# Kernel tuning notes

Hardware: AMD Instinct MI355X
Metric: run time of the kernel (lower is better)

## Reference

```python
import jax, jax.numpy as jnp
import numpy as np

B, T, C, H = 4, 1024, 1024, 16
HS = C // H  # head_size = 64
EPS = 1e-5


def layer_norm(x, w, b):
    mu = jnp.mean(x, axis=-1, keepdims=True)
    var = jnp.mean(jnp.square(x - mu), axis=-1, keepdims=True)
    return (x - mu) * jax.lax.rsqrt(var + EPS) * w + b


def setup_inputs() -> dict:
    key = jax.random.key(0)
    ks = jax.random.split(key, 12)
    s = 0.02
    return {
        "x": jax.random.normal(ks[0], (B, T, C), jnp.float32),
        "ln1_w": jnp.ones((C,), jnp.float32),
        "ln1_b": jnp.zeros((C,), jnp.float32),
        "Wk": jax.random.normal(ks[1], (H, C, HS), jnp.float32) * s,
        "Wq": jax.random.normal(ks[2], (H, C, HS), jnp.float32) * s,
        "Wv": jax.random.normal(ks[3], (H, C, HS), jnp.float32) * s,
        "Wo": jax.random.normal(ks[4], (C, C), jnp.float32) * s,
        "bo": jnp.zeros((C,), jnp.float32),
        "ln2_w": jnp.ones((C,), jnp.float32),
        "ln2_b": jnp.zeros((C,), jnp.float32),
        "W1": jax.random.normal(ks[5], (C, 4 * C), jnp.float32) * s,
        "b1": jnp.zeros((4 * C,), jnp.float32),
        "prelu_a": jnp.asarray(0.25, jnp.float32),
        "W2": jax.random.normal(ks[6], (4 * C, C), jnp.float32) * s,
        "b2": jnp.zeros((C,), jnp.float32),
    }


def reference(x, ln1_w, ln1_b, Wk, Wq, Wv, Wo, bo, ln2_w, ln2_b, W1, b1, prelu_a, W2, b2):
    # --- self-attention branch (pre-LN) ---
    h = layer_norm(x, ln1_w, ln1_b)  # [B,T,C]
    k = jnp.einsum('btc,hcd->bhtd', h, Wk)
    q = jnp.einsum('btc,hcd->bhtd', h, Wq)
    v = jnp.einsum('btc,hcd->bhtd', h, Wv)
    # NOTE: source computes k @ q^T (not q @ k^T) scaled by n_embd**-0.5
    wei = jnp.einsum('bhtd,bhsd->bhts', k, q) * (C ** -0.5)  # [B,H,T,T]
    causal = jnp.tril(jnp.ones((T, T), bool))
    wei = jnp.where(causal, wei, -jnp.inf)
    wei = jax.nn.softmax(wei, axis=-1)
    out = jnp.einsum('bhts,bhsd->bthd', wei, v).reshape(B, T, C)
    out = out @ Wo + bo
    x = x + out
    # --- feed-forward branch (pre-LN) ---
    h2 = layer_norm(x, ln2_w, ln2_b)
    f = h2 @ W1 + b1
    f = jnp.where(f > 0, f, prelu_a * f)  # PReLU, single scalar param
    f = f @ W2 + b2
    return x + f
```

## Files before the change

kernel.cpp:

```cpp
#include <hip/hip_runtime.h>


typedef __bf16 bf16_t;
typedef __attribute__((ext_vector_type(8))) __bf16 bfx8;
typedef __attribute__((ext_vector_type(4))) __bf16 bfx4;
typedef __attribute__((ext_vector_type(4))) float f32x4;
typedef __attribute__((ext_vector_type(8))) unsigned short u16x8;
typedef unsigned int u32;

#define MFMA_BF16(a, b, c) __builtin_amdgcn_mfma_f32_16x16x32_bf16((a), (b), (c), 0, 0, 0)
#define GLOAD_LDS16(g, l)                                                     \
  __builtin_amdgcn_global_load_lds((__attribute__((address_space(1))) void*)(g), \
                                   (__attribute__((address_space(3))) void*)(l), 16, 0, 0)

__global__ __launch_bounds__(256) void ln_kernel(const float* __restrict__ x,
                                                 const float* __restrict__ w,
                                                 const float* __restrict__ b,
                                                 bf16_t* __restrict__ out) {
  const int row = blockIdx.x;
  const int tid = threadIdx.x;
  const float4 v = reinterpret_cast<const float4*>(x + (size_t)row * 1024)[tid];
  float s = v.x + v.y + v.z + v.w;
  float s2 = v.x * v.x + v.y * v.y + v.z * v.z + v.w * v.w;
#pragma unroll
  for (int off = 1; off < 64; off <<= 1) {
    s += __shfl_xor(s, off);
    s2 += __shfl_xor(s2, off);
  }
  __shared__ float red[8];
  const int wv = tid >> 6;
  if ((tid & 63) == 0) {
    red[wv] = s;
    red[4 + wv] = s2;
  }
  __syncthreads();
  s = red[0] + red[1] + red[2] + red[3];
  s2 = red[4] + red[5] + red[6] + red[7];
  const float mu = s * (1.0f / 1024.0f);
  const float rs = rsqrtf(s2 * (1.0f / 1024.0f) - mu * mu + 1e-5f);
  const float4 wv4 = reinterpret_cast<const float4*>(w)[tid];
  const float4 bv4 = reinterpret_cast<const float4*>(b)[tid];
  bfx4 o;
  o[0] = (bf16_t)((v.x - mu) * rs * wv4.x + bv4.x);
  o[1] = (bf16_t)((v.y - mu) * rs * wv4.y + bv4.y);
  o[2] = (bf16_t)((v.z - mu) * rs * wv4.z + bv4.z);
  o[3] = (bf16_t)((v.w - mu) * rs * wv4.w + bv4.w);
  reinterpret_cast<bfx4*>(out + (size_t)row * 1024)[tid] = o;
}

__device__ __forceinline__ void tc_body(const float* __restrict__ in,
                                        bf16_t* __restrict__ out, int K, int N, int k0,
                                        int n0, float (*tile)[65], int t) {
  const int rl = t >> 4, cl = (t & 15) * 4;
#pragma unroll
  for (int p = 0; p < 4; ++p) {
    const int r = p * 16 + rl;
    const float4 v = *reinterpret_cast<const float4*>(in + (size_t)(k0 + r) * N + n0 + cl);
    tile[r][cl] = v.x;
    tile[r][cl + 1] = v.y;
    tile[r][cl + 2] = v.z;
    tile[r][cl + 3] = v.w;
  }
  __syncthreads();
#pragma unroll
  for (int p = 0; p < 2; ++p) {
    const int idx = p * 256 + t;
    const int n = idx >> 3, kc = (idx & 7) * 8;
    bfx8 o;
#pragma unroll
    for (int i = 0; i < 8; ++i) o[i] = (bf16_t)tile[kc + i][n];
    *reinterpret_cast<bfx8*>(out + (size_t)(n0 + n) * K + k0 + kc) = o;
  }
}

__global__ __launch_bounds__(256) void transpose_cast(const float* __restrict__ in,
                                                      bf16_t* __restrict__ out, int K,
                                                      int N) {
  __shared__ float tile[64][65];
  tc_body(in, out, K, N, blockIdx.x * 64, blockIdx.y * 64, tile, threadIdx.x);
}

__global__ __launch_bounds__(256) void transpose_qkv(const float* __restrict__ Wq,
                                                     const float* __restrict__ Wk,
                                                     const float* __restrict__ Wv,
                                                     bf16_t* __restrict__ out) {
  __shared__ float tile[64][65];
  const int z = blockIdx.y;
  const int sel = z >> 4, h = z & 15;
  const float* in = ((sel == 0) ? Wq : (sel == 1) ? Wk : Wv) + h * 65536;
  bf16_t* o = out + (size_t)sel * 1048576 + h * 65536;
  tc_body(in, o, 1024, 64, blockIdx.x * 64, 0, tile, threadIdx.x);
}

enum { EPI_QKV = 0, EPI_WO = 1, EPI_MLP1 = 2, EPI_FINAL = 3 };

template <int EPI, int BM, int BN, int NT>
__global__ __launch_bounds__(NT, 2) void gemm_bt(
    const bf16_t* __restrict__ A, const bf16_t* __restrict__ BT,
    const float* __restrict__ bias, const float* __restrict__ res,
    const float* __restrict__ prelu, float* __restrict__ outf,
    bf16_t* __restrict__ ob0, bf16_t* __restrict__ ob1, bf16_t* __restrict__ ob2,
    int K, int N) {
  constexpr int WM = 2;
  constexpr int WN = NT / 64 / WM;
  constexpr int MF = BM / WM / 16;
  constexpr int NF = BN / WN / 16;
  constexpr int ACH = BM * 64 / (NT * 8);
  constexpr int BCH = BN * 64 / (NT * 8);
  constexpr int LOADS = ACH + BCH;
  static_assert(LOADS == 8 || LOADS == 6, "add a vmcnt case");
  __shared__ __align__(16) bf16_t sA[2][BM * 64];
  __shared__ __align__(16) bf16_t sB[2][BN * 64];
  const int tid = threadIdx.x;
  const int lane = tid & 63;
  const int w = tid >> 6;
  const int wr = w / WN, wc = w % WN;
  const int g = lane >> 4, l15 = lane & 15;
  const int row0 = blockIdx.x * BM, col0 = blockIdx.y * BN;
  const int rowbase = row0 + wr * (BM / WM);
  const int colbase = wc * (BN / WN);

  f32x4 acc[MF][NF] = {};

  auto stage = [&](int k0, int buf) {
#pragma unroll
    for (int j = 0; j < ACH; ++j) {
      const int chunk = j * NT + tid;
      const int r = chunk >> 3, c = chunk & 7;
      GLOAD_LDS16(A + (size_t)(row0 + r) * K + k0 + ((c ^ (r & 7)) * 8),
                  sA[buf] + chunk * 8);
    }
#pragma unroll
    for (int j = 0; j < BCH; ++j) {
      const int chunk = j * NT + tid;
      const int r = chunk >> 3, c = chunk & 7;
      GLOAD_LDS16(BT + (size_t)(col0 + r) * K + k0 + ((c ^ (r & 7)) * 8),
                  sB[buf] + chunk * 8);
    }
  };

  stage(0, 0);
  const int nk = K >> 6;
  for (int t = 0; t < nk; ++t) {
    const int cur = t & 1;
    if (t + 1 < nk) {
      stage((t + 1) << 6, cur ^ 1);
      __builtin_amdgcn_sched_barrier(0);
      if constexpr (LOADS == 8)
        asm volatile("s_waitcnt vmcnt(8)");
      else
        asm volatile("s_waitcnt vmcnt(6)");
    } else {
      __builtin_amdgcn_sched_barrier(0);
      asm volatile("s_waitcnt vmcnt(0)");
    }
    __builtin_amdgcn_s_barrier();
    __builtin_amdgcn_sched_barrier(0);
    const bf16_t* __restrict__ pA = sA[cur];
    const bf16_t* __restrict__ pB = sB[cur];
#pragma unroll
    for (int kk = 0; kk < 2; ++kk) {
      bfx8 af[MF], bfr[NF];
#pragma unroll
      for (int m = 0; m < MF; ++m) {
        const int r = wr * (BM / WM) + m * 16 + l15;
        const int c = (kk * 4 + g) ^ (r & 7);
        af[m] = *reinterpret_cast<const bfx8*>(pA + r * 64 + c * 8);
      }
#pragma unroll
      for (int n = 0; n < NF; ++n) {
        const int r = colbase + n * 16 + l15;
        const int c = (kk * 4 + g) ^ (r & 7);
        bfr[n] = *reinterpret_cast<const bfx8*>(pB + r * 64 + c * 8);
      }
#pragma unroll
      for (int m = 0; m < MF; ++m)
#pragma unroll
        for (int n = 0; n < NF; ++n) acc[m][n] = MFMA_BF16(af[m], bfr[n], acc[m][n]);
    }
    __builtin_amdgcn_sched_barrier(0);
    __builtin_amdgcn_s_barrier();
  }

  const float pa = (EPI == EPI_MLP1) ? prelu[0] : 0.0f;
#pragma unroll
  for (int m = 0; m < MF; ++m) {
#pragma unroll
    for (int n = 0; n < NF; ++n) {
#pragma unroll
      for (int j = 0; j < 4; ++j) {
        const int row = rowbase + m * 16 + (g << 2) + j;
        const int col = col0 + colbase + n * 16 + l15;
        const float v = acc[m][n][j];
        if (EPI == EPI_QKV) {
          const int sel = col >> 10;
          const int h = (col >> 6) & 15, d = col & 63;
          const int bb = row >> 10, t = row & 1023;
          bf16_t* dst = (sel == 0) ? ob0 : (sel == 1) ? ob1 : ob2;
          dst[((size_t)(bb * 16 + h) * 1024 + t) * 64 + d] = (bf16_t)v;
        } else if (EPI == EPI_MLP1) {
          float t = v + bias[col];
          t = (t > 0.0f) ? t : pa * t;
          ob0[(size_t)row * N + col] = (bf16_t)t;
        } else {
          outf[(size_t)row * N + col] = v + bias[col] + res[(size_t)row * N + col];
        }
      }
    }
  }
}

__global__ __launch_bounds__(256) void attn_kernel(const bf16_t* __restrict__ kproj,
                                                   const bf16_t* __restrict__ qproj,
                                                   const bf16_t* __restrict__ vproj,
                                                   bf16_t* __restrict__ att) {
  __shared__ __align__(16) bf16_t sK[2][64 * 64];
  __shared__ __align__(16) bf16_t sVt[2][64 * 64];
  __shared__ __align__(16) bf16_t sP[4][16 * 64];
  const int tid = threadIdx.x, lane = tid & 63, w = tid >> 6;
  const int g = lane >> 4, l15 = lane & 15;
  const int bh = blockIdx.y;
  const size_t head = (size_t)bh * (1024 * 64);
  const int b = bh >> 4, h = bh & 15;
  const int vrow = 2 * (tid >> 3);
  const int vdb = tid & 7;

  for (int half = 0; half < 2; ++half) {
    const int tb = half ? (15 - (int)blockIdx.x) : (int)blockIdx.x;
    const int t0 = tb * 64;
    const int nsb = tb + 1;

    __syncthreads();

    bfx8 aq0, aq1;
    {
      const bf16_t* qrow = kproj + head + (size_t)(t0 + w * 16 + l15) * 64 + g * 8;
      aq0 = *reinterpret_cast<const bfx8*>(qrow);
      aq1 = *reinterpret_cast<const bfx8*>(qrow + 32);
    }

    {
#pragma unroll
      for (int j = 0; j < 2; ++j) {
        const int chunk = j * 256 + tid;
        const int r = chunk >> 3, c = chunk & 7;
        const int cs = c ^ (r & 7);
        GLOAD_LDS16(qproj + head + (size_t)r * 64 + cs * 8, sK[0] + chunk * 8);
      }
      const bf16_t* vp = vproj + head + (size_t)vrow * 64 + vdb * 8;
      const u16x8 v0 = *reinterpret_cast<const u16x8*>(vp);
      const u16x8 v1 = *reinterpret_cast<const u16x8*>(vp + 64);
#pragma unroll
      for (int i = 0; i < 8; ++i) {
        const int d = vdb * 8 + i;
        const int cc = ((vrow >> 3) ^ i ^ vdb) & 7;
        const u32 pk = ((u32)v1[i] << 16) | (u32)v0[i];
        *reinterpret_cast<u32*>(sVt[0] + d * 64 + cc * 8 + (vrow & 7)) = pk;
      }
    }
    __syncthreads();

    f32x4 accO[4] = {};
    float mrun[4], lrun[4];
#pragma unroll
    for (int j = 0; j < 4; ++j) {
      mrun[j] = -1e30f;
      lrun[j] = 0.0f;
    }

    for (int sb = 0; sb < nsb; ++sb) {
      const int cur = sb & 1;
      const bool pf = (sb + 1 < nsb);
      u16x8 v0n, v1n;
      if (pf) {
        const int s0n = (sb + 1) * 64;
#pragma unroll
        for (int j = 0; j < 2; ++j) {
          const int chunk = j * 256 + tid;
          const int r = chunk >> 3, c = chunk & 7;
          const int cs = c ^ (r & 7);
          GLOAD_LDS16(qproj + head + (size_t)(s0n + r) * 64 + cs * 8, sK[cur ^ 1] + chunk * 8);
        }
        const bf16_t* vp = vproj + head + (size_t)(s0n + vrow) * 64 + vdb * 8;
        v0n = *reinterpret_cast<const u16x8*>(vp);
        v1n = *reinterpret_cast<const u16x8*>(vp + 64);
      }

      f32x4 accS[4] = {};
      const bf16_t* sKc = sK[cur];
#pragma unroll
      for (int kk = 0; kk < 2; ++kk) {
        const bfx8 aq = kk ? aq1 : aq0;
#pragma unroll
        for (int n = 0; n < 4; ++n) {
          const int r = n * 16 + l15;
          const int c = (kk * 4 + g) ^ (r & 7);
          const bfx8 bk = *reinterpret_cast<const bfx8*>(sKc + r * 64 + c * 8);
          accS[n] = MFMA_BF16(aq, bk, accS[n]);
        }
      }

      const int rbase = t0 + w * 16 + (g << 2);
      const int cbase = sb * 64 + l15;
#pragma unroll
      for (int j = 0; j < 4; ++j) {
        const int t = rbase + j;
        float mx = -1e30f;
#pragma unroll
        for (int n = 0; n < 4; ++n) {
          float v = accS[n][j] * 0.03125f;
          v = ((cbase + n * 16) <= t) ? v : -1e30f;
          accS[n][j] = v;
          mx = fmaxf(mx, v);
        }
        mx = fmaxf(mx, __shfl_xor(mx, 1));
        mx = fmaxf(mx, __shfl_xor(mx, 2));
        mx = fmaxf(mx, __shfl_xor(mx, 4));
        mx = fmaxf(mx, __shfl_xor(mx, 8));
        const float mnew = fmaxf(mrun[j], mx);
        const float al = __expf(mrun[j] - mnew);
        float rsum = 0.0f;
#pragma unroll
        for (int n = 0; n < 4; ++n) {
          const float p = __expf(accS[n][j] - mnew);
          accS[n][j] = p;
          rsum += p;
        }
        rsum += __shfl_xor(rsum, 1);
        rsum += __shfl_xor(rsum, 2);
        rsum += __shfl_xor(rsum, 4);
        rsum += __shfl_xor(rsum, 8);
        lrun[j] = lrun[j] * al + rsum;
        mrun[j] = mnew;
#pragma unroll
        for (int n = 0; n < 4; ++n) accO[n][j] *= al;
      }

      bf16_t* sPw = sP[w];
#pragma unroll
      for (int n = 0; n < 4; ++n)
#pragma unroll
        for (int j = 0; j < 4; ++j) {
          const int r = (g << 2) + j;
          const int s = n * 16 + l15;
          const int cc = (s >> 3) ^ (r & 7);
          sPw[r * 64 + cc * 8 + (s & 7)] = (bf16_t)accS[n][j];
        }

      const bf16_t* sVc = sVt[cur];
#pragma unroll
      for (int kk = 0; kk < 2; ++kk) {
        bfx8 ap;
        {
          const int r = l15;
          const int c = (kk * 4 + g) ^ (r & 7);
          ap = *reinterpret_cast<const bfx8*>(sPw + r * 64 + c * 8);
        }
#pragma unroll
        for (int n = 0; n < 4; ++n) {
          const int d = n * 16 + l15;
          const int c = (kk * 4 + g) ^ (d & 7) ^ ((d >> 3) & 7);
          const bfx8 bv = *reinterpret_cast<const bfx8*>(sVc + d * 64 + c * 8);
          accO[n] = MFMA_BF16(ap, bv, accO[n]);
        }
      }

      if (pf) {
#pragma unroll
        for (int i = 0; i < 8; ++i) {
          const int d = vdb * 8 + i;
          const int cc = ((vrow >> 3) ^ i ^ vdb) & 7;
          const u32 pk = ((u32)v1n[i] << 16) | (u32)v0n[i];
          *reinterpret_cast<u32*>(sVt[cur ^ 1] + d * 64 + cc * 8 + (vrow & 7)) = pk;
        }
      }
      __syncthreads();
    }

#pragma unroll
    for (int j = 0; j < 4; ++j) {
      const float inv = 1.0f / lrun[j];
      const int t = t0 + w * 16 + (g << 2) + j;
#pragma unroll
      for (int n = 0; n < 4; ++n) {
        const int d = n * 16 + l15;
        att[((size_t)(b * 1024 + t)) * 1024 + h * 64 + d] = (bf16_t)(accO[n][j] * inv);
      }
    }
  }
}

extern "C" void kernel_launch(void* const* d_in, const int* in_sizes, int n_in,
                              void* d_out, int out_size, void* d_ws, size_t ws_size,
                              hipStream_t stream) {
  (void)in_sizes; (void)n_in; (void)out_size; (void)ws_size;
  const float* x = (const float*)d_in[0];
  const float* ln1w = (const float*)d_in[1];
  const float* ln1b = (const float*)d_in[2];
  const float* Wk = (const float*)d_in[3];
  const float* Wq = (const float*)d_in[4];
  const float* Wv = (const float*)d_in[5];
  const float* Wo = (const float*)d_in[6];
  const float* bo = (const float*)d_in[7];
  const float* ln2w = (const float*)d_in[8];
  const float* ln2b = (const float*)d_in[9];
  const float* W1 = (const float*)d_in[10];
  const float* b1 = (const float*)d_in[11];
  const float* pa = (const float*)d_in[12];
  const float* W2 = (const float*)d_in[13];
  const float* b2 = (const float*)d_in[14];
  float* out = (float*)d_out;
  char* ws = (char*)d_ws;
  const size_t MB = 1ull << 20;
  bf16_t* h1 = (bf16_t*)(ws + 0 * MB);
  bf16_t* h2 = (bf16_t*)(ws + 8 * MB);
  bf16_t* qb = (bf16_t*)(ws + 16 * MB);
  bf16_t* kb = (bf16_t*)(ws + 24 * MB);
  bf16_t* vb = (bf16_t*)(ws + 32 * MB);
  bf16_t* attb = (bf16_t*)(ws + 40 * MB);
  bf16_t* fbuf = (bf16_t*)(ws + 48 * MB);
  bf16_t* WqkvT = (bf16_t*)(ws + 80 * MB);
  bf16_t* WoT = (bf16_t*)(ws + 86 * MB);
  bf16_t* W1T = (bf16_t*)(ws + 88 * MB);
  bf16_t* W2T = (bf16_t*)(ws + 96 * MB);

  transpose_qkv<<<dim3(16, 48), 256, 0, stream>>>(Wq, Wk, Wv, WqkvT);
  transpose_cast<<<dim3(16, 16), 256, 0, stream>>>(Wo, WoT, 1024, 1024);
  transpose_cast<<<dim3(16, 64), 256, 0, stream>>>(W1, W1T, 1024, 4096);
  transpose_cast<<<dim3(64, 16), 256, 0, stream>>>(W2, W2T, 4096, 1024);

  ln_kernel<<<4096, 256, 0, stream>>>(x, ln1w, ln1b, h1);
  gemm_bt<EPI_QKV, 256, 256, 512><<<dim3(16, 12), 512, 0, stream>>>(
      h1, WqkvT, nullptr, nullptr, nullptr, nullptr, qb, kb, vb, 1024, 3072);
  attn_kernel<<<dim3(8, 64), 256, 0, stream>>>(kb, qb, vb, attb);
  gemm_bt<EPI_WO, 64, 128, 256><<<dim3(64, 8), 256, 0, stream>>>(
      attb, WoT, bo, x, nullptr, out, nullptr, nullptr, nullptr, 1024, 1024);
  ln_kernel<<<4096, 256, 0, stream>>>(out, ln2w, ln2b, h2);
  gemm_bt<EPI_MLP1, 256, 256, 512><<<dim3(16, 16), 512, 0, stream>>>(
      h2, W1T, b1, nullptr, pa, nullptr, fbuf, nullptr, nullptr, 1024, 4096);
  gemm_bt<EPI_FINAL, 64, 128, 256><<<dim3(64, 8), 256, 0, stream>>>(
      fbuf, W2T, b2, out, nullptr, out, nullptr, nullptr, nullptr, 4096, 1024);
}
```

Measured before the change: 226.6 us.

## Add eight-phase pipelined GEMM kernel for MLP1 with fine-grained staging

Replaces the generic double-buffered GEMM used for the MLP up-projection with a dedicated 256x256 kernel. The kernel splits each K=64 tile into four quadrant MFMA phases and interleaves half-tile global-to-LDS loads between them, separated by barriers and wait counts. It also raises MFMA priority with setprio. The aim is to overlap memory traffic with compute more finely than the two-stage loop did. It adds a memory clobber to existing waitcnt asm and many barriers per iteration, and the hand-written ordering of stages is easy to get wrong.

```diff
diff --git a/kernel.cpp b/kernel.cpp
--- a/kernel.cpp
+++ b/kernel.cpp
@@ -12,6 +12,15 @@
 #define GLOAD_LDS16(g, l)                                                     \
   __builtin_amdgcn_global_load_lds((__attribute__((address_space(1))) void*)(g), \
                                    (__attribute__((address_space(3))) void*)(l), 16, 0, 0)
+#define BARX()                      \
+  __builtin_amdgcn_s_barrier();     \
+  __builtin_amdgcn_sched_barrier(0)
+#define VMW6()                                     \
+  asm volatile("s_waitcnt vmcnt(6)" ::: "memory"); \
+  __builtin_amdgcn_sched_barrier(0)
+#define VMW0()                                     \
+  asm volatile("s_waitcnt vmcnt(0)" ::: "memory"); \
+  __builtin_amdgcn_sched_barrier(0)
 
 __global__ __launch_bounds__(256) void ln_kernel(const float* __restrict__ x,
                                                  const float* __restrict__ w,
@@ -147,12 +156,12 @@
       stage((t + 1) << 6, cur ^ 1);
       __builtin_amdgcn_sched_barrier(0);
       if constexpr (LOADS == 8)
-        asm volatile("s_waitcnt vmcnt(8)");
+        asm volatile("s_waitcnt vmcnt(8)" ::: "memory");
       else
-        asm volatile("s_waitcnt vmcnt(6)");
+        asm volatile("s_waitcnt vmcnt(6)" ::: "memory");
     } else {
       __builtin_amdgcn_sched_barrier(0);
-      asm volatile("s_waitcnt vmcnt(0)");
+      asm volatile("s_waitcnt vmcnt(0)" ::: "memory");
     }
     __builtin_amdgcn_s_barrier();
     __builtin_amdgcn_sched_barrier(0);
@@ -205,6 +214,142 @@
         } else {
           outf[(size_t)row * N + col] = v + bias[col] + res[(size_t)row * N + col];
         }
+      }
+    }
+  }
+}
+
+__device__ __forceinline__ void stageA8(const bf16_t* __restrict__ A, int K, int row0,
+                                        int k0, int mh, bf16_t* dst, int tid) {
+#pragma unroll
+  for (int g2 = 0; g2 < 2; ++g2) {
+    const int band = g2 * 128 + mh * 64;
+    const int row = band + (tid >> 3);
+    GLOAD_LDS16(A + (size_t)(row0 + row) * K + k0 + (((tid & 7) ^ (row & 7)) * 8),
+                dst + band * 64 + tid * 8);
+  }
+}
+
+__device__ __forceinline__ void stageB8(const bf16_t* __restrict__ BT, int K, int col0,
+                                        int k0, int nh, bf16_t* dst, int tid) {
+#pragma unroll
+  for (int g2 = 0; g2 < 2; ++g2) {
+    const int rho = g2 * 64 + (tid >> 3);
+    const int grow = (rho >> 5) * 64 + nh * 32 + (rho & 31);
+    GLOAD_LDS16(BT + (size_t)(col0 + grow) * K + k0 + (((tid & 7) ^ (rho & 7)) * 8),
+                dst + nh * 8192 + g2 * 4096 + tid * 8);
+  }
+}
+
+template <int MH, int NH, bool LOADA>
+__device__ __forceinline__ void quad8(const bf16_t* __restrict__ pA,
+                                      const bf16_t* __restrict__ pB, int wr, int wc,
+                                      int l15, int g, bfx8 (&af)[4][2],
+                                      f32x4 (&acc)[8][4]) {
+  if (LOADA) {
+#pragma unroll
+    for (int i = 0; i < 4; ++i) {
+      const int r = wr * 128 + (MH * 4 + i) * 16 + l15;
+#pragma unroll
+      for (int kk = 0; kk < 2; ++kk)
+        af[i][kk] =
+            *reinterpret_cast<const bfx8*>(pA + r * 64 + (((kk * 4 + g) ^ (r & 7)) * 8));
+    }
+  }
+  bfx8 bfr[2][2];
+#pragma unroll
+  for (int i = 0; i < 2; ++i) {
+    const int rho = wc * 32 + i * 16 + l15;
+#pragma unroll
+    for (int kk = 0; kk < 2; ++kk)
+      bfr[i][kk] = *reinterpret_cast<const bfx8*>(pB + NH * 8192 + rho * 64 +
+                                                  (((kk * 4 + g) ^ (rho & 7)) * 8));
+  }
+  __builtin_amdgcn_s_setprio(1);
+#pragma unroll
+  for (int i = 0; i < 4; ++i)
+#pragma unroll
+    for (int jn = 0; jn < 2; ++jn)
+#pragma unroll
+      for (int kk = 0; kk < 2; ++kk)
+        acc[MH * 4 + i][NH * 2 + jn] =
+            MFMA_BF16(af[i][kk], bfr[jn][kk], acc[MH * 4 + i][NH * 2 + jn]);
+  __builtin_amdgcn_s_setprio(0);
+}
+
+__global__ __launch_bounds__(512, 2) void gemm_8ph_mlp1(
+    const bf16_t* __restrict__ A, const bf16_t* __restrict__ BT,
+    const float* __restrict__ bias, const float* __restrict__ prelu,
+    bf16_t* __restrict__ outb, int K, int N) {
+  __shared__ __align__(16) bf16_t sA[2][256 * 64];
+  __shared__ __align__(16) bf16_t sB[2][256 * 64];
+  const int tid = threadIdx.x;
+  const int lane = tid & 63;
+  const int w = tid >> 6;
+  const int wr = w >> 2, wc = w & 3;
+  const int g = lane >> 4, l15 = lane & 15;
+  const int row0 = blockIdx.x * 256, col0 = blockIdx.y * 256;
+
+  f32x4 acc[8][4] = {};
+  bfx8 af[4][2];
+
+  stageA8(A, K, row0, 0, 0, sA[0], tid);
+  stageB8(BT, K, col0, 0, 0, sB[0], tid);
+  stageB8(BT, K, col0, 0, 1, sB[0], tid);
+  stageA8(A, K, row0, 0, 1, sA[0], tid);
+  stageA8(A, K, row0, 64, 0, sA[1], tid);
+  stageB8(BT, K, col0, 64, 0, sB[1], tid);
+
+  const int nt = K >> 7;
+  for (int j = 0; j < nt; ++j) {
+    const bool more = (j + 1 < nt);
+    const int ku1 = (2 * j + 1) << 6, k2 = (2 * j + 2) << 6, k3 = (2 * j + 3) << 6;
+    BARX();
+    stageB8(BT, K, col0, ku1, 1, sB[1], tid);
+    VMW6();
+    BARX();
+    quad8<0, 0, true>(sA[0], sB[0], wr, wc, l15, g, af, acc);
+    BARX();
+    stageA8(A, K, row0, ku1, 1, sA[1], tid);
+    quad8<0, 1, false>(sA[0], sB[0], wr, wc, l15, g, af, acc);
+    BARX();
+    if (more) stageA8(A, K, row0, k2, 0, sA[0], tid);
+    quad8<1, 0, true>(sA[0], sB[0], wr, wc, l15, g, af, acc);
+    BARX();
+    if (more) stageB8(BT, K, col0, k2, 0, sB[0], tid);
+    quad8<1, 1, false>(sA[0], sB[0], wr, wc, l15, g, af, acc);
+    BARX();
+    if (more) {
+      stageB8(BT, K, col0, k2, 1, sB[0], tid);
+      VMW6();
+    } else {
+      VMW0();
+    }
+    BARX();
+    quad8<0, 0, true>(sA[1], sB[1], wr, wc, l15, g, af, acc);
+    BARX();
+    if (more) stageA8(A, K, row0, k2, 1, sA[0], tid);
+    quad8<0, 1, false>(sA[1], sB[1], wr, wc, l15, g, af, acc);
+    BARX();
+    if (more) stageA8(A, K, row0, k3, 0, sA[1], tid);
+    quad8<1, 0, true>(sA[1], sB[1], wr, wc, l15, g, af, acc);
+    BARX();
+    if (more) stageB8(BT, K, col0, k3, 0, sB[1], tid);
+    quad8<1, 1, false>(sA[1], sB[1], wr, wc, l15, g, af, acc);
+  }
+
+  const float pa = prelu[0];
+#pragma unroll
+  for (int m = 0; m < 8; ++m) {
+#pragma unroll
+    for (int n = 0; n < 4; ++n) {
+#pragma unroll
+      for (int j = 0; j < 4; ++j) {
+        const int row = row0 + wr * 128 + m * 16 + (g << 2) + j;
+        const int col = col0 + wc * 64 + n * 16 + l15;
+        float t = acc[m][n][j] + bias[col];
+        t = (t > 0.0f) ? t : pa * t;
+        outb[(size_t)row * N + col] = (bf16_t)t;
       }
     }
   }
@@ -436,8 +581,7 @@
   gemm_bt<EPI_WO, 64, 128, 256><<<dim3(64, 8), 256, 0, stream>>>(
       attb, WoT, bo, x, nullptr, out, nullptr, nullptr, nullptr, 1024, 1024);
   ln_kernel<<<4096, 256, 0, stream>>>(out, ln2w, ln2b, h2);
-  gemm_bt<EPI_MLP1, 256, 256, 512><<<dim3(16, 16), 512, 0, stream>>>(
-      h2, W1T, b1, nullptr, pa, nullptr, fbuf, nullptr, nullptr, 1024, 4096);
+  gemm_8ph_mlp1<<<dim3(16, 16), 512, 0, stream>>>(h2, W1T, b1, pa, fbuf, 1024, 4096);
   gemm_bt<EPI_FINAL, 64, 128, 256><<<dim3(64, 8), 256, 0, stream>>>(
       fbuf, W2T, b2, out, nullptr, out, nullptr, nullptr, nullptr, 4096, 1024);
 }
```

New measurement: 225.3 us. About the same (-0.6%).
